# Performance work log

Measured on AMD Instinct MI355X. Metric: run time of the kernel, lower is better.

## Reference

```python
import jax, jax.numpy as jnp
import numpy as np

KS = 3      # kernel size
PAD = 1     # zero padding
STRIDE = 1
N = KS * KS # 9 sampling points per pixel


def _deform_conv(feature, offset, weight):
    """DeformConv2d: bilinear sample at learned offsets then 3x3 conv (no bias)."""
    b, c, h, w = feature.shape
    x = jnp.pad(feature, ((0, 0), (0, 0), (PAD, PAD), (PAD, PAD)))
    hp, wp = h + 2 * PAD, w + 2 * PAD
    dt = feature.dtype
    # p_n: kernel grid offsets, x(rows) first then y(cols) -> (2N,)
    rng = jnp.arange(-(KS - 1) // 2, (KS - 1) // 2 + 1, dtype=dt)
    pn_x, pn_y = jnp.meshgrid(rng, rng, indexing='ij')
    # p_0: base sampling grid starting at 1 (accounts for zero padding)
    p0_x, p0_y = jnp.meshgrid(jnp.arange(1, h + 1, dtype=dt),
                              jnp.arange(1, w + 1, dtype=dt), indexing='ij')
    # sampling locations p = p_0 + p_n + offset, split into x/y -> (b,h,w,N)
    off = jnp.transpose(offset, (0, 2, 3, 1))  # (b,h,w,2N)
    px = p0_x[None, :, :, None] + pn_x.reshape(-1)[None, None, None, :] + off[..., :N]
    py = p0_y[None, :, :, None] + pn_y.reshape(-1)[None, None, None, :] + off[..., N:]
    q_lt_x = jnp.clip(jnp.floor(px), 0, hp - 1)
    q_lt_y = jnp.clip(jnp.floor(py), 0, wp - 1)
    q_rb_x = jnp.clip(jnp.floor(px) + 1, 0, hp - 1)
    q_rb_y = jnp.clip(jnp.floor(py) + 1, 0, wp - 1)
    px = jnp.clip(px, 0, hp - 1)
    py = jnp.clip(py, 0, wp - 1)
    # bilinear weights for the 4 corners
    g_lt = (1 + (q_lt_x - px)) * (1 + (q_lt_y - py))
    g_rb = (1 - (q_rb_x - px)) * (1 - (q_rb_y - py))
    g_lb = (1 + (q_lt_x - px)) * (1 - (q_rb_y - py))
    g_rt = (1 - (q_rb_x - px)) * (1 + (q_lt_y - py))
    x_flat = x.reshape(b, c, hp * wp)

    def gather(qx, qy):
        idx = (qx * wp + qy).astype(jnp.int32).reshape(b, 1, -1)
        v = jnp.take_along_axis(x_flat, jnp.broadcast_to(idx, (b, c, h * w * N)), axis=2)
        return v.reshape(b, c, h, w, N)

    x_off = (g_lt[:, None] * gather(q_lt_x, q_lt_y)
             + g_rb[:, None] * gather(q_rb_x, q_rb_y)
             + g_lb[:, None] * gather(q_lt_x, q_rb_y)
             + g_rt[:, None] * gather(q_rb_x, q_lt_y))  # (b,c,h,w,N)
    # equivalent of _reshape_x_offset + conv(ks, stride=ks)
    x_off = x_off.reshape(b, c, h, w, KS, KS)
    return jnp.einsum('bchwij,ocij->bohw', x_off, weight)


def setup_inputs() -> dict:
    key = jax.random.key(0)
    k1, k2, k3 = jax.random.split(key, 3)
    B, C, H, W = 4, 256, 64, 64
    feature = jax.random.normal(k1, (B, C, H, W), dtype=jnp.float32)
    offset = jax.random.normal(k2, (B, 2 * N, H, W), dtype=jnp.float32)
    weight = jax.random.normal(k3, (C, C, KS, KS), dtype=jnp.float32) / np.sqrt(C * N)
    return {"feature": feature, "offset": offset, "weight": weight}


def reference(feature, offset, weight):
    f1 = jax.nn.relu(_deform_conv(feature, offset, weight))
    return jax.nn.relu(f1 + feature)
```

## Files before the change

kernel.cpp:

```cpp
#include <hip/hip_runtime.h>

#define HW    4096
#define J_TOT 16384
#define K_TOT 2304
#define C_CH  256

typedef unsigned short u16;
typedef unsigned int   u32;
typedef __attribute__((ext_vector_type(8))) short short8;
typedef __attribute__((ext_vector_type(4))) float f32x4;
typedef __attribute__((ext_vector_type(8))) unsigned short us8;

__device__ __forceinline__ float b2f(u16 u) { return __uint_as_float(((u32)u) << 16); }
__device__ __forceinline__ u16 f2b(float x) {
  u32 u = __float_as_uint(x);
  u += 0x7FFFu + ((u >> 16) & 1u);
  return (u16)(u >> 16);
}

__device__ __forceinline__ void gload_lds16(const u16* g, u16* l) {
  __builtin_amdgcn_global_load_lds(
      (__attribute__((address_space(1))) void*)(void*)g,
      (__attribute__((address_space(3))) void*)(void*)l, 16, 0, 0);
}

__global__ void k_detect(const u16* __restrict__ f, int* __restrict__ flag) {
  __shared__ int sh[256];
  int t = threadIdx.x;
  int hits = 0;
  for (int i = t; i < 2048; i += 256) {
    u16 u = f[2 * i];
    int e = (u >> 7) & 0xFF;
    hits += (e >= 100 && e <= 141) ? 1 : 0;
  }
  sh[t] = hits;
  __syncthreads();
  if (t == 0) {
    int s = 0;
    for (int i = 0; i < 256; i++) s += sh[i];
    flag[0] = (s > 1024) ? 1 : 0;
  }
}

__global__ void k_prep(const void* __restrict__ featv, u16* __restrict__ ftr,
                       const void* __restrict__ wv, u16* __restrict__ Wr,
                       const int* __restrict__ flag) {
  int isbf = *flag;
  int tx = threadIdx.x;
  int ty = threadIdx.y;
  int z = blockIdx.z;
  if (z < 4) {
    __shared__ u16 tile[32][33];
    int b = z;
    int hw0 = blockIdx.x << 5;
    int c0 = blockIdx.y << 5;
    if (isbf) {
      const u16* f = (const u16*)featv;
#pragma unroll
      for (int i = 0; i < 4; i++) {
        int c = c0 + ty + i * 8;
        tile[ty + i * 8][tx] = f[(((size_t)(b * C_CH + c)) << 12) + hw0 + tx];
      }
    } else {
      const float* f = (const float*)featv;
#pragma unroll
      for (int i = 0; i < 4; i++) {
        int c = c0 + ty + i * 8;
        tile[ty + i * 8][tx] = f2b(f[(((size_t)(b * C_CH + c)) << 12) + hw0 + tx]);
      }
    }
    __syncthreads();
#pragma unroll
    for (int i = 0; i < 4; i++) {
      int hw = hw0 + ty + i * 8;
      ftr[(((size_t)(b * HW + hw)) << 8) + c0 + tx] = tile[tx][ty + i * 8];
    }
  } else {
    int bid = blockIdx.x + (blockIdx.y << 7);
    int flat = ty * 32 + tx;
    for (int idx = bid * 256 + flat; idx < C_CH * K_TOT; idx += 1024 * 256) {
      int c = idx & 255;
      int n = (idx >> 8) % 9;
      int o = idx / K_TOT;
      int src = (o * 256 + c) * 9 + n;
      if (isbf) Wr[idx] = ((const u16*)wv)[src];
      else      Wr[idx] = f2b(((const float*)wv)[src]);
    }
  }
}

#define NT 36

#define A_DMA(bufi)                                                          \
  do {                                                                       \
    gload_lds16(asrc0, &As[bufi][wave * 1024]);                              \
    gload_lds16(asrc1, &As[bufi][wave * 1024 + 512]);                        \
    asrc0 += 64; asrc1 += 64;                                                \
  } while (0)

#define PLOAD(tile)                                                          \
  do {                                                                       \
    int np = (tile) >> 2, c0 = ((tile) & 3) << 6;                            \
    w0 = gs[np][0][pp]; w1 = gs[np][1][pp];                                  \
    w2 = gs[np][2][pp]; w3 = gs[np][3][pp];                                  \
    q0 = *(const us8*)(ftr + isx[np][0][pp] + c0 + cb8);                     \
    q1 = *(const us8*)(ftr + isx[np][1][pp] + c0 + cb8);                     \
    q2 = *(const us8*)(ftr + isx[np][2][pp] + c0 + cb8);                     \
    q3 = *(const us8*)(ftr + isx[np][3][pp] + c0 + cb8);                     \
  } while (0)

#define PFIN(bufi)                                                           \
  do {                                                                       \
    us8 ov;                                                                  \
    _Pragma("unroll")                                                        \
    for (int i = 0; i < 8; i++) {                                            \
      float v = w0 * b2f(q0[i]) + w1 * b2f(q1[i]) +                          \
                w2 * b2f(q2[i]) + w3 * b2f(q3[i]);                           \
      ov[i] = f2b(v);                                                        \
    }                                                                        \
    *(us8*)(&Bs[bufi][bofs]) = ov;                                           \
  } while (0)

#define GEMM_COMPUTE(bufi)                                                   \
  do {                                                                       \
    short8 af[2][2], bf[2][2];                                               \
    _Pragma("unroll")                                                        \
    for (int kk = 0; kk < 2; kk++) {                                         \
      int go = (((kk << 2) + lk) ^ swz) << 3;                                \
      _Pragma("unroll")                                                      \
      for (int oi = 0; oi < 2; oi++)                                         \
        af[oi][kk] = *(const short8*)(As[bufi] + (wo * 32 + oi * 16 + lr) * 64 + go); \
      _Pragma("unroll")                                                      \
      for (int ji = 0; ji < 2; ji++)                                         \
        bf[ji][kk] = *(const short8*)(Bs[bufi] + (wj * 32 + ji * 16 + lr) * 64 + go); \
    }                                                                        \
    __builtin_amdgcn_s_setprio(1);                                           \
    _Pragma("unroll")                                                        \
    for (int kk = 0; kk < 2; kk++)                                           \
      _Pragma("unroll")                                                      \
      for (int oi = 0; oi < 2; oi++)                                         \
        _Pragma("unroll")                                                    \
        for (int ji = 0; ji < 2; ji++)                                       \
          acc[oi][ji] = __builtin_amdgcn_mfma_f32_16x16x32_bf16(             \
              af[oi][kk], bf[ji][kk], acc[oi][ji], 0, 0, 0);                 \
    __builtin_amdgcn_s_setprio(0);                                           \
  } while (0)

__global__ __launch_bounds__(512) void k_gemm(const u16* __restrict__ Wr,
                                              const u16* __restrict__ ftr,
                                              const void* __restrict__ offv,
                                              const void* __restrict__ featv,
                                              void* __restrict__ outv,
                                              const int* __restrict__ flag) {
  __shared__ u16 As[2][128 * 64];
  __shared__ u16 Bs[2][64 * 64];
  __shared__ float gs[9][4][64];
  __shared__ int   isx[9][4][64];
  int isbf = *flag;
  int j0 = blockIdx.x << 6;
  int ob0 = blockIdx.y << 7;
  int b = j0 >> 12;
  int hw0 = j0 & (HW - 1);
  int t = threadIdx.x;
  int wave = t >> 6, lane = t & 63;
  int wj = wave >> 2, wo = wave & 3;
  int lr = lane & 15, lk = lane >> 4;
  int swz = lr & 7;

  for (int e = t; e < 576; e += 512) {
    int n = e >> 6, p = e & 63;
    int hw = hw0 + p;
    int h = hw >> 6, w = hw & 63;
    size_t obi = (((size_t)(b * 18 + n)) << 12) + hw;
    float ox, oy;
    if (isbf) {
      const u16* po = (const u16*)offv;
      ox = b2f(po[obi]);
      oy = b2f(po[obi + (9u << 12)]);
    } else {
      const float* po = (const float*)offv;
      ox = po[obi];
      oy = po[obi + (9u << 12)];
    }
    int ki = n / 3, kj = n % 3;
    float px = (float)(h + ki) + ox;
    float py = (float)(w + kj) + oy;
    float fx = floorf(px), fy = floorf(py);
    float qltx = fminf(fmaxf(fx, 0.f), 65.f);
    float qlty = fminf(fmaxf(fy, 0.f), 65.f);
    float qrbx = fminf(fmaxf(fx + 1.f, 0.f), 65.f);
    float qrby = fminf(fmaxf(fy + 1.f, 0.f), 65.f);
    float pcx = fminf(fmaxf(px, 0.f), 65.f);
    float pcy = fminf(fmaxf(py, 0.f), 65.f);
    float dltx = 1.f + (qltx - pcx);
    float drbx = 1.f - (qrbx - pcx);
    float dlty = 1.f + (qlty - pcy);
    float drby = 1.f - (qrby - pcy);
    float g0 = dltx * dlty;
    float g1 = drbx * drby;
    float g2 = dltx * drby;
    float g3 = drbx * dlty;
    int x0 = (int)qltx, y0 = (int)qlty, x1 = (int)qrbx, y1 = (int)qrby;
    int v0 = (x0 >= 1 && x0 <= 64 && y0 >= 1 && y0 <= 64);
    int v1 = (x1 >= 1 && x1 <= 64 && y1 >= 1 && y1 <= 64);
    int v2 = (x0 >= 1 && x0 <= 64 && y1 >= 1 && y1 <= 64);
    int v3 = (x1 >= 1 && x1 <= 64 && y0 >= 1 && y0 <= 64);
    int base = b << 12;
    isx[n][0][p] = v0 ? ((base + ((x0 - 1) << 6) + (y0 - 1)) << 8) : 0;
    isx[n][1][p] = v1 ? ((base + ((x1 - 1) << 6) + (y1 - 1)) << 8) : 0;
    isx[n][2][p] = v2 ? ((base + ((x0 - 1) << 6) + (y1 - 1)) << 8) : 0;
    isx[n][3][p] = v3 ? ((base + ((x1 - 1) << 6) + (y0 - 1)) << 8) : 0;
    gs[n][0][p] = v0 ? g0 : 0.f;
    gs[n][1][p] = v1 ? g1 : 0.f;
    gs[n][2][p] = v2 ? g2 : 0.f;
    gs[n][3][p] = v3 ? g3 : 0.f;
  }

  f32x4 acc[2][2];
  f32x4 zero = {0.f, 0.f, 0.f, 0.f};
#pragma unroll
  for (int i = 0; i < 2; i++)
#pragma unroll
    for (int j = 0; j < 2; j++) acc[i][j] = zero;

  int rb = lane >> 3;
  int cs = ((lane & 7) ^ rb) << 3;
  const u16* asrc0 = Wr + (size_t)(ob0 + wave * 16 + 0 + rb) * K_TOT + cs;
  const u16* asrc1 = Wr + (size_t)(ob0 + wave * 16 + 8 + rb) * K_TOT + cs;

  int pp = t >> 3, cg = t & 7;
  int bofs = pp * 64 + ((cg ^ (pp & 7)) << 3);
  int cb8 = cg << 3;

  __syncthreads();

  us8 q0, q1, q2, q3;
  float w0, w1, w2, w3;

  PLOAD(0);
  A_DMA(0);
  PFIN(0);
  __syncthreads();

  for (int tt = 0; tt < NT - 1; ++tt) {
    int cbuf = tt & 1, nbuf = cbuf ^ 1;
    PLOAD(tt + 1);
    A_DMA(nbuf);
    GEMM_COMPUTE(cbuf);
    PFIN(nbuf);
    __syncthreads();
  }
  GEMM_COMPUTE((NT - 1) & 1);

  int lq = lane >> 4;
#pragma unroll
  for (int oi = 0; oi < 2; oi++) {
#pragma unroll
    for (int ji = 0; ji < 2; ji++) {
      int j = j0 + wj * 32 + ji * 16 + lr;
      int bb_ = j >> 12, hw = j & (HW - 1);
      int o0 = ob0 + wo * 32 + oi * 16 + lq * 4;
#pragma unroll
      for (int r = 0; r < 4; r++) {
        size_t oidx = (((size_t)(bb_ * C_CH + o0 + r)) << 12) + hw;
        float v = acc[oi][ji][r];
        v = fmaxf(v, 0.f);
        float ft = isbf ? b2f(((const u16*)featv)[oidx]) : ((const float*)featv)[oidx];
        v = fmaxf(v + ft, 0.f);
        if (isbf) ((u16*)outv)[oidx] = f2b(v);
        else      ((float*)outv)[oidx] = v;
      }
    }
  }
}

extern "C" void kernel_launch(void* const* d_in, const int* in_sizes, int n_in,
                              void* d_out, int out_size, void* d_ws, size_t ws_size,
                              hipStream_t stream) {
  const void* feat = d_in[0];
  const void* offs = d_in[1];
  const void* wght = d_in[2];

  const size_t off_flag = 0;
  const size_t off_wr   = 256;
  const size_t off_ftr  = off_wr + (size_t)1179648;
  const size_t need     = off_ftr + (size_t)8388608;
  if (ws_size < need) return;

  char* ws = (char*)d_ws;
  int* flag = (int*)(ws + off_flag);
  u16* Wr   = (u16*)(ws + off_wr);
  u16* ftr  = (u16*)(ws + off_ftr);

  k_detect<<<1, 256, 0, stream>>>((const u16*)feat, flag);
  k_prep<<<dim3(128, 8, 5), dim3(32, 8), 0, stream>>>(feat, ftr, wght, Wr, flag);
  k_gemm<<<dim3(J_TOT / 64, 2), 512, 0, stream>>>(Wr, ftr, offs, feat, d_out, flag);
}
```

Before: 136.4 us.

## Compute all output channels per block to avoid duplicate bilinear gathers

Each block now covers all 256 output channels with 1024 threads (16 waves), where before the output-channel dimension was split across two blocks. The bilinear sampling and interpolation of the deformable input tile is therefore done once per pixel tile instead of twice. Each thread now gathers and interpolates 4 channels instead of 8. The trade-offs are double the LDS for the weight tile, half as many blocks in the grid, and a launch-bounds change that could press on registers.

```diff
diff --git a/kernel.cpp b/kernel.cpp
--- a/kernel.cpp
+++ b/kernel.cpp
@@ -10,6 +10,7 @@
 typedef __attribute__((ext_vector_type(8))) short short8;
 typedef __attribute__((ext_vector_type(4))) float f32x4;
 typedef __attribute__((ext_vector_type(8))) unsigned short us8;
+typedef __attribute__((ext_vector_type(4))) unsigned short us4;
 
 __device__ __forceinline__ float b2f(u16 u) { return __uint_as_float(((u32)u) << 16); }
 __device__ __forceinline__ u16 f2b(float x) {
@@ -103,22 +104,22 @@
     int np = (tile) >> 2, c0 = ((tile) & 3) << 6;                            \
     w0 = gs[np][0][pp]; w1 = gs[np][1][pp];                                  \
     w2 = gs[np][2][pp]; w3 = gs[np][3][pp];                                  \
-    q0 = *(const us8*)(ftr + isx[np][0][pp] + c0 + cb8);                     \
-    q1 = *(const us8*)(ftr + isx[np][1][pp] + c0 + cb8);                     \
-    q2 = *(const us8*)(ftr + isx[np][2][pp] + c0 + cb8);                     \
-    q3 = *(const us8*)(ftr + isx[np][3][pp] + c0 + cb8);                     \
+    q0 = *(const us4*)(ftr + isx[np][0][pp] + c0 + cb4);                     \
+    q1 = *(const us4*)(ftr + isx[np][1][pp] + c0 + cb4);                     \
+    q2 = *(const us4*)(ftr + isx[np][2][pp] + c0 + cb4);                     \
+    q3 = *(const us4*)(ftr + isx[np][3][pp] + c0 + cb4);                     \
   } while (0)
 
 #define PFIN(bufi)                                                           \
   do {                                                                       \
-    us8 ov;                                                                  \
+    us4 ov;                                                                  \
     _Pragma("unroll")                                                        \
-    for (int i = 0; i < 8; i++) {                                            \
+    for (int i = 0; i < 4; i++) {                                            \
       float v = w0 * b2f(q0[i]) + w1 * b2f(q1[i]) +                          \
                 w2 * b2f(q2[i]) + w3 * b2f(q3[i]);                           \
       ov[i] = f2b(v);                                                        \
     }                                                                        \
-    *(us8*)(&Bs[bufi][bofs]) = ov;                                           \
+    *(us4*)(&Bs[bufi][bofs]) = ov;                                           \
   } while (0)
 
 #define GEMM_COMPUTE(bufi)                                                   \
@@ -146,29 +147,28 @@
     __builtin_amdgcn_s_setprio(0);                                           \
   } while (0)
 
-__global__ __launch_bounds__(512) void k_gemm(const u16* __restrict__ Wr,
-                                              const u16* __restrict__ ftr,
-                                              const void* __restrict__ offv,
-                                              const void* __restrict__ featv,
-                                              void* __restrict__ outv,
-                                              const int* __restrict__ flag) {
-  __shared__ u16 As[2][128 * 64];
+__global__ __launch_bounds__(1024, 4) void k_gemm(const u16* __restrict__ Wr,
+                                                  const u16* __restrict__ ftr,
+                                                  const void* __restrict__ offv,
+                                                  const void* __restrict__ featv,
+                                                  void* __restrict__ outv,
+                                                  const int* __restrict__ flag) {
+  __shared__ u16 As[2][256 * 64];
   __shared__ u16 Bs[2][64 * 64];
   __shared__ float gs[9][4][64];
   __shared__ int   isx[9][4][64];
   int isbf = *flag;
   int j0 = blockIdx.x << 6;
-  int ob0 = blockIdx.y << 7;
   int b = j0 >> 12;
   int hw0 = j0 & (HW - 1);
   int t = threadIdx.x;
   int wave = t >> 6, lane = t & 63;
-  int wj = wave >> 2, wo = wave & 3;
+  int wj = wave >> 3, wo = wave & 7;
   int lr = lane & 15, lk = lane >> 4;
   int swz = lr & 7;
 
-  for (int e = t; e < 576; e += 512) {
-    int n = e >> 6, p = e & 63;
+  if (t < 576) {
+    int n = t >> 6, p = t & 63;
     int hw = hw0 + p;
     int h = hw >> 6, w = hw & 63;
     size_t obi = (((size_t)(b * 18 + n)) << 12) + hw;
@@ -225,16 +225,17 @@
 
   int rb = lane >> 3;
   int cs = ((lane & 7) ^ rb) << 3;
-  const u16* asrc0 = Wr + (size_t)(ob0 + wave * 16 + 0 + rb) * K_TOT + cs;
-  const u16* asrc1 = Wr + (size_t)(ob0 + wave * 16 + 8 + rb) * K_TOT + cs;
-
-  int pp = t >> 3, cg = t & 7;
-  int bofs = pp * 64 + ((cg ^ (pp & 7)) << 3);
-  int cb8 = cg << 3;
+  const u16* asrc0 = Wr + (size_t)(wave * 16 + 0 + rb) * K_TOT + cs;
+  const u16* asrc1 = Wr + (size_t)(wave * 16 + 8 + rb) * K_TOT + cs;
+
+  int pp = t >> 4, qq = t & 15;
+  int cgp = qq >> 1, half = qq & 1;
+  int bofs = pp * 64 + ((cgp ^ (pp & 7)) << 3) + (half << 2);
+  int cb4 = (cgp << 3) + (half << 2);
 
   __syncthreads();
 
-  us8 q0, q1, q2, q3;
+  us4 q0, q1, q2, q3;
   float w0, w1, w2, w3;
 
   PLOAD(0);
@@ -259,7 +260,7 @@
     for (int ji = 0; ji < 2; ji++) {
       int j = j0 + wj * 32 + ji * 16 + lr;
       int bb_ = j >> 12, hw = j & (HW - 1);
-      int o0 = ob0 + wo * 32 + oi * 16 + lq * 4;
+      int o0 = wo * 32 + oi * 16 + lq * 4;
 #pragma unroll
       for (int r = 0; r < 4; r++) {
         size_t oidx = (((size_t)(bb_ * C_CH + o0 + r)) << 12) + hw;
@@ -294,5 +295,5 @@
 
   k_detect<<<1, 256, 0, stream>>>((const u16*)feat, flag);
   k_prep<<<dim3(128, 8, 5), dim3(32, 8), 0, stream>>>(feat, ftr, wght, Wr, flag);
-  k_gemm<<<dim3(J_TOT / 64, 2), 512, 0, stream>>>(Wr, ftr, offs, feat, d_out, flag);
-}
+  k_gemm<<<J_TOT / 64, 1024, 0, stream>>>(Wr, ftr, offs, feat, d_out, flag);
+}
```

New measurement: 136.1 us. No clear change (-0.2%).
